# Kernel tuning notes

Hardware: AMD Instinct MI355X
Metric: run time of the kernel (lower is better)

The kernel has to match this reference:

```python
import jax, jax.numpy as jnp
import numpy as np

# Model dims: E experts, T total routed tokens, D model dim, H expert hidden dim
E, T, D, H = 8, 16384, 2048, 5632


def setup_inputs() -> dict:
    key = jax.random.key(0)
    k1, k2, k3, k4 = jax.random.split(key, 4)
    init_std = 0.02
    x = jax.random.normal(k1, (T, D), dtype=jnp.float32)
    # w1/w3: (num_experts, hidden_dim, dim); w2: (num_experts, dim, hidden_dim)
    w1 = jax.random.normal(k2, (E, H, D), dtype=jnp.float32) * init_std
    w2 = jax.random.normal(k3, (E, D, H), dtype=jnp.float32) * init_std
    w3 = jax.random.normal(k4, (E, H, D), dtype=jnp.float32) * init_std
    # Tokens are pre-sorted by expert; even split so sum == T (no padding path)
    num_tokens_per_expert = jnp.full((E,), T // E, dtype=jnp.int32)
    return {"x": x, "w1": w1, "w2": w2, "w3": w3,
            "num_tokens_per_expert": num_tokens_per_expert}


def reference(x, w1, w2, w3, num_tokens_per_expert):
    """Grouped-GEMM SwiGLU experts: out[t] = silu(x@w1[e].T) * (x@w3[e].T) @ w2[e].T
    where e is the expert owning token t (tokens sorted by expert).
    lax.ragged_dot is the exact grouped-GEMM primitive: lhs (m,k), rhs (g,k,n),
    group_sizes (g,) -> (m,n). Weights are stored as (g, out, in), so swap to (g, in, out),
    matching the torch matmul with transpose(-2, -1).
    """
    groups = num_tokens_per_expert.astype(jnp.int32)
    gate = jax.lax.ragged_dot(x, jnp.swapaxes(w1, 1, 2), groups)   # (T, H)
    up = jax.lax.ragged_dot(x, jnp.swapaxes(w3, 1, 2), groups)     # (T, H)
    h = jax.nn.silu(gate) * up                                      # fused SwiGLU
    out = jax.lax.ragged_dot(h, jnp.swapaxes(w2, 1, 2), groups)    # (T, D)
    return out
```

## Files before the change

### kernel.cpp

```cpp
#include <hip/hip_runtime.h>
#include <hip/hip_bf16.h>


typedef __bf16 bf16x8 __attribute__((ext_vector_type(8)));
typedef float f32x4 __attribute__((ext_vector_type(4)));
typedef unsigned short u16x8 __attribute__((ext_vector_type(8)));

constexpr int E = 8;
constexpr int T = 16384;
constexpr int D = 2048;
constexpr int H = 5632;

#define DEV static __device__ __forceinline__

DEV unsigned short f2bf(float f) {
    unsigned u = __builtin_bit_cast(unsigned, f);
    u = (u + 0x7FFFu + ((u >> 16) & 1u)) >> 16;
    return (unsigned short)u;
}

DEV void gload16(const void* g, void* l) {
    __builtin_amdgcn_global_load_lds(
        (const __attribute__((address_space(1))) void*)g,
        (__attribute__((address_space(3))) void*)l, 16, 0, 0);
}

DEV f32x4 mfma16(bf16x8 a, bf16x8 b, f32x4 c) {
    return __builtin_amdgcn_mfma_f32_16x16x32_bf16(a, b, c, 0, 0, 0);
}

DEV void cvt8(const float* src, unsigned short* dst) {
    float4 a = *(const float4*)src;
    float4 c = *(const float4*)(src + 4);
    u16x8 r;
    r[0] = f2bf(a.x); r[1] = f2bf(a.y); r[2] = f2bf(a.z); r[3] = f2bf(a.w);
    r[4] = f2bf(c.x); r[5] = f2bf(c.y); r[6] = f2bf(c.z); r[7] = f2bf(c.w);
    *(u16x8*)dst = r;
}

__global__ __launch_bounds__(256) void k_cvt(const float* __restrict__ in,
                                             unsigned short* __restrict__ out,
                                             long n8) {
    long i = (long)blockIdx.x * blockDim.x + threadIdx.x;
    long stride = (long)gridDim.x * blockDim.x;
    for (; i < n8; i += stride) cvt8(in + i * 8, out + i * 8);
}

__global__ __launch_bounds__(256) void k_cvt_w13(
    const float* __restrict__ in, unsigned short* __restrict__ out,
    int which) {
    const long n8 = (long)E * H * D / 8;
    long i = (long)blockIdx.x * blockDim.x + threadIdx.x;
    long stride = (long)gridDim.x * blockDim.x;
    for (; i < n8; i += stride) {
        int col8 = (int)(i & 255);
        int row = (int)(i >> 8);
        int e = row / H;
        int h = row - e * H;
        int rr = ((h >> 4) << 5) + (which << 4) + (h & 15);
        cvt8(in + i * 8,
             out + ((size_t)e * (2 * H) + rr) * D + (size_t)col8 * 8);
    }
}

DEV int expert_of_row(const int* __restrict__ ntp, int row0) {
    int e = 0, s = 0;
    for (int i = 0; i < E; ++i) {
        int c = ntp[i];
        if (row0 < s + c) { e = i; break; }
        s += c;
    }
    return e;
}

template <int LD, int NT>
DEV void gemm_4p(const unsigned short* pa, const unsigned short* pb,
                 unsigned short* sA, unsigned short* sB, int tid,
                 f32x4 (&acc)[8][4]) {
    const int lane = tid & 63, wid = tid >> 6;
    const int wm = wid >> 2, wn = wid & 3;

    const int q8 = (((lane >> 4) ^ ((lane >> 1) & 3)) << 3);
    const int aoff = (wm * 128 + (lane & 15)) * 32 + q8;
    const int boff = (wn * 64 + (lane & 15)) * 32 + q8;

    char* lA = (char*)sA;
    char* lB = (char*)sB;
    const int dW = wid << 10;

    auto stA = [&](int t, int kk) {
        const unsigned short* g = pa + (size_t)t * 64 + kk * 32;
        char* l = lA + ((t & 1) << 15) + (kk << 14) + dW;
        gload16(g, l);
        gload16(g + (size_t)128 * LD, l + 8192);
    };
    auto stB = [&](int t, int kk) {
        const unsigned short* g = pb + (size_t)t * 64 + kk * 32;
        char* l = lB + ((t & 1) << 15) + (kk << 14) + dW;
        gload16(g, l);
        gload16(g + (size_t)128 * LD, l + 8192);
    };

    stA(0, 0); stB(0, 0); stA(0, 1); stB(0, 1);
    asm volatile("s_waitcnt vmcnt(4)" ::: "memory");
    __builtin_amdgcn_s_barrier();

#pragma unroll 1
    for (int t = 0; t < NT; ++t) {
        const int sb = (t & 1) << 14;
        const unsigned short* A0 = sA + sb + aoff;
        const unsigned short* B0 = sB + sb + boff;
        const unsigned short* A1 = A0 + 8192;
        const unsigned short* B1 = B0 + 8192;
        const bool more = (t + 1 < NT);
        bf16x8 a[4], b[4];

#pragma unroll
        for (int i = 0; i < 4; ++i) a[i] = *(const bf16x8*)(A0 + i * 512);
#pragma unroll
        for (int i = 0; i < 4; ++i) b[i] = *(const bf16x8*)(B0 + i * 512);
        if (more) stA(t + 1, 0);
        __builtin_amdgcn_s_barrier();
        asm volatile("s_waitcnt lgkmcnt(0)" ::: "memory");
        __builtin_amdgcn_sched_barrier(0);
        __builtin_amdgcn_s_setprio(1);
#pragma unroll
        for (int m = 0; m < 4; ++m)
#pragma unroll
            for (int n = 0; n < 4; ++n)
                acc[m][n] = mfma16(a[m], b[n], acc[m][n]);
        __builtin_amdgcn_s_setprio(0);
        __builtin_amdgcn_s_barrier();

#pragma unroll
        for (int i = 0; i < 4; ++i)
            a[i] = *(const bf16x8*)(A0 + 2048 + i * 512);
        if (more) {
            stB(t + 1, 0);
            asm volatile("s_waitcnt vmcnt(4)" ::: "memory");
        } else {
            asm volatile("s_waitcnt vmcnt(0)" ::: "memory");
        }
        __builtin_amdgcn_s_barrier();
        asm volatile("s_waitcnt lgkmcnt(0)" ::: "memory");
        __builtin_amdgcn_sched_barrier(0);
        __builtin_amdgcn_s_setprio(1);
#pragma unroll
        for (int m = 0; m < 4; ++m)
#pragma unroll
            for (int n = 0; n < 4; ++n)
                acc[4 + m][n] = mfma16(a[m], b[n], acc[4 + m][n]);
        __builtin_amdgcn_s_setprio(0);
        __builtin_amdgcn_s_barrier();

#pragma unroll
        for (int i = 0; i < 4; ++i) a[i] = *(const bf16x8*)(A1 + i * 512);
#pragma unroll
        for (int i = 0; i < 4; ++i) b[i] = *(const bf16x8*)(B1 + i * 512);
        if (more) stA(t + 1, 1);
        __builtin_amdgcn_s_barrier();
        asm volatile("s_waitcnt lgkmcnt(0)" ::: "memory");
        __builtin_amdgcn_sched_barrier(0);
        __builtin_amdgcn_s_setprio(1);
#pragma unroll
        for (int m = 0; m < 4; ++m)
#pragma unroll
            for (int n = 0; n < 4; ++n)
                acc[m][n] = mfma16(a[m], b[n], acc[m][n]);
        __builtin_amdgcn_s_setprio(0);
        __builtin_amdgcn_s_barrier();

#pragma unroll
        for (int i = 0; i < 4; ++i)
            a[i] = *(const bf16x8*)(A1 + 2048 + i * 512);
        if (more) {
            stB(t + 1, 1);
            asm volatile("s_waitcnt vmcnt(4)" ::: "memory");
        }
        __builtin_amdgcn_s_barrier();
        asm volatile("s_waitcnt lgkmcnt(0)" ::: "memory");
        __builtin_amdgcn_sched_barrier(0);
        __builtin_amdgcn_s_setprio(1);
#pragma unroll
        for (int m = 0; m < 4; ++m)
#pragma unroll
            for (int n = 0; n < 4; ++n)
                acc[4 + m][n] = mfma16(a[m], b[n], acc[4 + m][n]);
        __builtin_amdgcn_s_setprio(0);
        __builtin_amdgcn_s_barrier();
    }
}

__global__ __launch_bounds__(512, 2) void k_gate_up(
    const unsigned short* __restrict__ xb,
    const unsigned short* __restrict__ w13b,
    const int* __restrict__ ntp,
    unsigned short* __restrict__ hbuf) {
    __shared__ unsigned short sA[2 * 2 * 8192];
    __shared__ unsigned short sB[2 * 2 * 8192];

    const int nwg = gridDim.x;
    const int cpx = nwg >> 3;
    const int bid = blockIdx.x;
    const int swz = (bid & 7) * cpx + (bid >> 3);
    const int tm = swz & 63;
    const int tn = swz >> 6;

    const int row0 = tm << 8;
    const int e = expert_of_row(ntp, row0);
    const int tid = threadIdx.x;
    const int lane = tid & 63, wid = tid >> 6;

    const int srow = tid >> 2;
    const int sq = (tid & 3) ^ ((tid >> 3) & 3);
    const unsigned short* pa = xb + (size_t)(row0 + srow) * D + sq * 8;
    const unsigned short* pb = w13b + (size_t)e * (2 * H) * D +
                               (size_t)((tn << 8) + srow) * D + sq * 8;

    f32x4 acc[8][4] = {};
    gemm_4p<D, D / 64>(pa, pb, sA, sB, tid, acc);

    const int wm = wid >> 2, wn = wid & 3;
    const int rbase = row0 + (wm << 7) + ((lane >> 4) << 2);
    const int cb = (((tn << 3) + (wn << 1)) << 4) + (lane & 15);
#pragma unroll
    for (int mi = 0; mi < 8; ++mi)
#pragma unroll
        for (int pi = 0; pi < 2; ++pi) {
            f32x4 g = acc[mi][2 * pi], u = acc[mi][2 * pi + 1];
            const int hcol = cb + (pi << 4);
#pragma unroll
            for (int j = 0; j < 4; ++j) {
                float gv = g[j];
                float hv = gv * u[j] / (1.f + __expf(-gv));
                hbuf[(size_t)(rbase + (mi << 4) + j) * H + hcol] = f2bf(hv);
            }
        }
}

__global__ __launch_bounds__(512, 2) void k_down(
    const unsigned short* __restrict__ hbuf,
    const unsigned short* __restrict__ w2b,
    const int* __restrict__ ntp,
    float* __restrict__ out) {
    __shared__ unsigned short sA[2 * 2 * 8192];
    __shared__ unsigned short sB[2 * 2 * 8192];

    const int nwg = gridDim.x;
    const int cpx = nwg >> 3;
    const int bid = blockIdx.x;
    const int swz = (bid & 7) * cpx + (bid >> 3);
    const int tm = swz & 63;
    const int tn = swz >> 6;

    const int row0 = tm << 8;
    const int e = expert_of_row(ntp, row0);
    const int tid = threadIdx.x;
    const int lane = tid & 63, wid = tid >> 6;

    const int srow = tid >> 2;
    const int sq = (tid & 3) ^ ((tid >> 3) & 3);
    const unsigned short* pa = hbuf + (size_t)(row0 + srow) * H + sq * 8;
    const unsigned short* pb = w2b + (size_t)e * D * H +
                               (size_t)((tn << 8) + srow) * H + sq * 8;

    f32x4 acc[8][4] = {};
    gemm_4p<H, H / 64>(pa, pb, sA, sB, tid, acc);

    const int wm = wid >> 2, wn = wid & 3;
    const int rbase = row0 + (wm << 7) + ((lane >> 4) << 2);
    const int cb = (tn << 8) + (wn << 6) + (lane & 15);
#pragma unroll
    for (int mi = 0; mi < 8; ++mi)
#pragma unroll
        for (int ni = 0; ni < 4; ++ni) {
            f32x4 c = acc[mi][ni];
#pragma unroll
            for (int j = 0; j < 4; ++j)
                out[(size_t)(rbase + (mi << 4) + j) * D + cb + (ni << 4)] =
                    c[j];
        }
}

extern "C" void kernel_launch(void* const* d_in, const int* in_sizes, int n_in,
                              void* d_out, int out_size, void* d_ws,
                              size_t ws_size, hipStream_t stream) {
    const float* x = (const float*)d_in[0];
    const float* w1 = (const float*)d_in[1];
    const float* w2 = (const float*)d_in[2];
    const float* w3 = (const float*)d_in[3];
    const int* ntp = (const int*)d_in[4];
    float* out = (float*)d_out;

    char* ws = (char*)d_ws;
    unsigned short* xb = (unsigned short*)(ws + 0);
    unsigned short* w13b = (unsigned short*)(ws + 67108864L);
    unsigned short* hbuf = (unsigned short*)(ws + 67108864L + 385875968L);
    unsigned short* w2b = w13b;

    k_cvt<<<2048, 256, 0, stream>>>(x, xb, (long)T * D / 8);
    k_cvt_w13<<<2048, 256, 0, stream>>>(w1, w13b, 0);
    k_cvt_w13<<<2048, 256, 0, stream>>>(w3, w13b, 1);

    k_gate_up<<<(T / 256) * (2 * H / 256), 512, 0, stream>>>(xb, w13b, ntp,
                                                             hbuf);

    k_cvt<<<2048, 256, 0, stream>>>(w2, w2b, (long)E * D * H / 8);

    k_down<<<(T / 256) * (D / 256), 512, 0, stream>>>(hbuf, w2b, ntp, out);
}
```

Measured before the change: 1.465 ms.

## Fuse input conversions into one kernel and fold w2 conversion into gate/up GEMM

Merges the x, w1 and w3 fp32-to-bf16 conversions into a single launch, partitioned by block ranges. When the workspace is large enough, w2 gets its own buffer and each gate/up GEMM block converts one slice of w2 before its matmul, removing the separate w2 conversion launch. This aims to cut launch overhead and hide conversion traffic among GEMM work. The cost is a conversion prologue at the start of every GEMM block, which delays the tiles' compute and adds memory pressure.

```diff
diff --git a/kernel.cpp b/kernel.cpp
--- a/kernel.cpp
+++ b/kernel.cpp
@@ -38,29 +38,38 @@
     *(u16x8*)dst = r;
 }
 
+__global__ __launch_bounds__(256) void k_cvt_pre(
+    const float* __restrict__ x, const float* __restrict__ w1,
+    const float* __restrict__ w3, unsigned short* __restrict__ xb,
+    unsigned short* __restrict__ w13b) {
+    const int bid = blockIdx.x, tid = threadIdx.x;
+    if (bid < 512) {
+        const long n8 = (long)T * D / 8;
+        for (long i = (long)bid * 256 + tid; i < n8; i += 512L * 256)
+            cvt8(x + i * 8, xb + i * 8);
+    } else {
+        const int which = (bid < 1280) ? 0 : 1;
+        const float* src = which ? w3 : w1;
+        const long b0 = which ? 1280 : 512;
+        const long n8 = (long)E * H * D / 8;
+        for (long i = ((long)bid - b0) * 256 + tid; i < n8; i += 768L * 256) {
+            int col8 = (int)(i & 255);
+            int rowi = (int)(i >> 8);
+            int e = rowi / H;
+            int h = rowi - e * H;
+            int rr = ((h >> 4) << 5) + (which << 4) + (h & 15);
+            cvt8(src + i * 8,
+                 w13b + ((size_t)e * (2 * H) + rr) * D + (size_t)col8 * 8);
+        }
+    }
+}
+
 __global__ __launch_bounds__(256) void k_cvt(const float* __restrict__ in,
                                              unsigned short* __restrict__ out,
                                              long n8) {
     long i = (long)blockIdx.x * blockDim.x + threadIdx.x;
     long stride = (long)gridDim.x * blockDim.x;
     for (; i < n8; i += stride) cvt8(in + i * 8, out + i * 8);
-}
-
-__global__ __launch_bounds__(256) void k_cvt_w13(
-    const float* __restrict__ in, unsigned short* __restrict__ out,
-    int which) {
-    const long n8 = (long)E * H * D / 8;
-    long i = (long)blockIdx.x * blockDim.x + threadIdx.x;
-    long stride = (long)gridDim.x * blockDim.x;
-    for (; i < n8; i += stride) {
-        int col8 = (int)(i & 255);
-        int row = (int)(i >> 8);
-        int e = row / H;
-        int h = row - e * H;
-        int rr = ((h >> 4) << 5) + (which << 4) + (h & 15);
-        cvt8(in + i * 8,
-             out + ((size_t)e * (2 * H) + rr) * D + (size_t)col8 * 8);
-    }
 }
 
 DEV int expert_of_row(const int* __restrict__ ntp, int row0) {
@@ -194,28 +203,37 @@
 __global__ __launch_bounds__(512, 2) void k_gate_up(
     const unsigned short* __restrict__ xb,
     const unsigned short* __restrict__ w13b,
-    const int* __restrict__ ntp,
-    unsigned short* __restrict__ hbuf) {
+    const float* __restrict__ w2, unsigned short* __restrict__ w2b,
+    const int* __restrict__ ntp, unsigned short* __restrict__ hbuf) {
     __shared__ unsigned short sA[2 * 2 * 8192];
     __shared__ unsigned short sB[2 * 2 * 8192];
 
-    const int nwg = gridDim.x;
-    const int cpx = nwg >> 3;
     const int bid = blockIdx.x;
-    const int swz = (bid & 7) * cpx + (bid >> 3);
-    const int tm = swz & 63;
-    const int tn = swz >> 6;
+    const int tid = threadIdx.x;
+
+    if (w2) {
+        const float* src = w2 + (size_t)bid * 32768;
+        unsigned short* dst = w2b + (size_t)bid * 32768;
+#pragma unroll
+        for (int it = 0; it < 8; ++it) {
+            int o = (it * 512 + tid) * 8;
+            cvt8(src + o, dst + o);
+        }
+        asm volatile("s_waitcnt vmcnt(0)" ::: "memory");
+    }
+
+    const int tm = (bid & 7) * 8 + ((bid >> 3) & 7);
+    const int tn = bid >> 6;
 
     const int row0 = tm << 8;
     const int e = expert_of_row(ntp, row0);
-    const int tid = threadIdx.x;
     const int lane = tid & 63, wid = tid >> 6;
 
-    const int srow = tid >> 2;
+    const int sr = tid >> 2;
     const int sq = (tid & 3) ^ ((tid >> 3) & 3);
-    const unsigned short* pa = xb + (size_t)(row0 + srow) * D + sq * 8;
+    const unsigned short* pa = xb + (size_t)(row0 + sr) * D + sq * 8;
     const unsigned short* pb = w13b + (size_t)e * (2 * H) * D +
-                               (size_t)((tn << 8) + srow) * D + sq * 8;
+                               (size_t)((tn << 8) + sr) * D + sq * 8;
 
     f32x4 acc[8][4] = {};
     gemm_4p<D, D / 64>(pa, pb, sA, sB, tid, acc);
@@ -258,11 +276,11 @@
     const int tid = threadIdx.x;
     const int lane = tid & 63, wid = tid >> 6;
 
-    const int srow = tid >> 2;
+    const int sr = tid >> 2;
     const int sq = (tid & 3) ^ ((tid >> 3) & 3);
-    const unsigned short* pa = hbuf + (size_t)(row0 + srow) * H + sq * 8;
+    const unsigned short* pa = hbuf + (size_t)(row0 + sr) * H + sq * 8;
     const unsigned short* pb = w2b + (size_t)e * D * H +
-                               (size_t)((tn << 8) + srow) * H + sq * 8;
+                               (size_t)((tn << 8) + sr) * H + sq * 8;
 
     f32x4 acc[8][4] = {};
     gemm_4p<H, H / 64>(pa, pb, sA, sB, tid, acc);
@@ -295,17 +313,17 @@
     char* ws = (char*)d_ws;
     unsigned short* xb = (unsigned short*)(ws + 0);
     unsigned short* w13b = (unsigned short*)(ws + 67108864L);
-    unsigned short* hbuf = (unsigned short*)(ws + 67108864L + 385875968L);
-    unsigned short* w2b = w13b;
-
-    k_cvt<<<2048, 256, 0, stream>>>(x, xb, (long)T * D / 8);
-    k_cvt_w13<<<2048, 256, 0, stream>>>(w1, w13b, 0);
-    k_cvt_w13<<<2048, 256, 0, stream>>>(w3, w13b, 1);
-
-    k_gate_up<<<(T / 256) * (2 * H / 256), 512, 0, stream>>>(xb, w13b, ntp,
-                                                             hbuf);
-
-    k_cvt<<<2048, 256, 0, stream>>>(w2, w2b, (long)E * D * H / 8);
+    unsigned short* hbuf = (unsigned short*)(ws + 436207616L);
+    const bool big = ws_size >= 805306368UL;
+    unsigned short* w2b = big ? (unsigned short*)(ws + 620756992L) : w13b;
+
+    k_cvt_pre<<<2048, 256, 0, stream>>>(x, w1, w3, xb, w13b);
+
+    k_gate_up<<<(T / 256) * (2 * H / 256), 512, 0, stream>>>(
+        xb, w13b, big ? w2 : nullptr, big ? w2b : nullptr, ntp, hbuf);
+
+    if (!big)
+        k_cvt<<<2048, 256, 0, stream>>>(w2, w2b, (long)E * D * H / 8);
 
     k_down<<<(T / 256) * (D / 256), 512, 0, stream>>>(hbuf, w2b, ntp, out);
 }
```

After: 1.416 ms. 1.03x faster.
